# Performance work log

Measured on AMD Instinct MI355X. Metric: run time of the kernel, lower is better.

The kernel has to match this reference:

```python
import jax, jax.numpy as jnp
import numpy as np

B_, N, P, HID, KT = 1, 2048, 9, 32, 3
N_AGG = 7
AVG_LOG_DEG = 7.625  # info.deg: dataset-average log(degree+1) used by PNA scalers
EPS = 1e-8


def _adj_mats(A):
    # Precompute per-adjacency aggregation matrices (shared across b, p, c).
    mask = A > 0
    degb = jnp.maximum(jnp.sum(mask, axis=-1).astype(A.dtype), 1.0)  # [n]
    Wb = mask.astype(A.dtype) / degb[:, None]                        # binary mean
    Wa = A / (jnp.sum(A, axis=-1, keepdims=True) + EPS)              # distance-weighted mean
    neg = jnp.asarray(-1e9, A.dtype)
    Sp = jax.nn.softmax(jnp.where(mask, A, neg), axis=-1)            # softmax agg weights
    Sm = jax.nn.softmax(jnp.where(mask, -A, neg), axis=-1)           # softmin agg weights
    return Wb, Wa, Sp, Sm, degb


def spatial_conv(X, A, theta, bias, use_scalers):
    # X: [b, c, n, p]  ->  out: [b, o, n, p]
    h = jnp.transpose(X, (0, 3, 2, 1))  # [b, p, n, c]
    Wb, Wa, Sp, Sm, degb = _adj_mats(A)
    agg = lambda M, Y: jnp.einsum('nm,bpmc->bpnc', M, Y)
    h2 = h * h
    mean_b = agg(Wb, h)
    mean_a = agg(Wa, h)
    var_b = jnp.maximum(agg(Wb, h2) - mean_b * mean_b, 0.0)
    var_a = jnp.maximum(agg(Wa, h2) - mean_a * mean_a, 0.0)
    out = jnp.concatenate([
        agg(Sm, h),             # softmin
        agg(Sp, h),             # softmax
        mean_b,                 # normalized_mean
        jnp.sqrt(var_b + EPS),  # std
        var_b,                  # var
        mean_a,                 # distance
        jnp.sqrt(var_a + EPS),  # d_std
    ], axis=3)                  # [b, p, n, 7c]
    if use_scalers:
        s = (jnp.log(degb + 1.0) / AVG_LOG_DEG)[None, None, :, None]
        out = jnp.concatenate([out, out * s, out / s], axis=3)  # identity/amp/atten
    out = jnp.einsum('bpnc,co->bpno', out, theta) + bias
    out = jnp.transpose(out, (0, 3, 2, 1))  # [b, o, n, p]
    return jax.nn.leaky_relu(out, 0.01)     # dropout is a no-op at inference


def conv_t(X, w, b):
    # X: [b, c, n, p]; w: [o, i, 1, k]; 'same' padding along time dim
    y = jax.lax.conv_general_dilated(X, w, (1, 1), 'SAME',
                                     dimension_numbers=('NCHW', 'OIHW', 'NCHW'))
    return y + b[None, :, None, None]


def setup_inputs() -> dict:
    key = jax.random.key(0)
    ks = jax.random.split(key, 16)

    def xavier(k, shape):
        lim = np.sqrt(6.0 / (shape[0] + shape[1]))
        return jax.random.uniform(k, shape, jnp.float32, -lim, lim)

    stdv = 1.0 / np.sqrt(HID)
    return {
        'X': jax.random.normal(ks[0], (B_, 1, N, P), jnp.float32),
        'A_first': jax.random.uniform(ks[1], (N, N), jnp.float32),
        'A_sub': jax.random.uniform(ks[2], (N, N), jnp.float32),
        'coords': jax.random.uniform(ks[3], (N, 2), jnp.float32),
        'theta0': xavier(ks[4], (N_AGG * 1 * 1, HID)),
        'bias0': jax.random.uniform(ks[5], (HID,), jnp.float32, -stdv, stdv),
        'tconv0_w': jax.random.normal(ks[6], (2 * HID, HID, 1, KT), jnp.float32) * 0.05,
        'tconv0_b': jnp.zeros((2 * HID,), jnp.float32),
        'theta1': xavier(ks[7], (N_AGG * 3 * HID, HID)),
        'bias1': jax.random.uniform(ks[8], (HID,), jnp.float32, -stdv, stdv),
        'tconv1_w': jax.random.normal(ks[9], (HID, HID, 1, KT), jnp.float32) * 0.05,
        'tconv1_b': jnp.zeros((HID,), jnp.float32),
        'out_conv_w': jax.random.normal(ks[10], (1, HID, 1, 1), jnp.float32) * 0.1,
        'out_conv_b': jnp.zeros((1,), jnp.float32),
        'out_lin_w': jax.random.normal(ks[11], (P, P), jnp.float32) * 0.1,  # torch Linear [out,in]
        'out_lin_b': jnp.zeros((P,), jnp.float32),
    }


def reference(X, A_first, A_sub, coords, theta0, bias0, tconv0_w, tconv0_b,
              theta1, bias1, tconv1_w, tconv1_b, out_conv_w, out_conv_b,
              out_lin_w, out_lin_b):
    # pe_size=0 -> PositionalEncoding is identity (coords unused)
    h = spatial_conv(X, A_first, theta0, bias0, use_scalers=False)  # s_conv0, scalers=['identity']
    # t_conv0: GLU temporal conv; in_size == out_size so align is identity
    o = conv_t(h, tconv0_w, tconv0_b)
    h = (o[:, :HID] + h) * jax.nn.sigmoid(o[:, HID:])
    # layers from spec 'STSTr'[2:] = 'ST'
    h = spatial_conv(h, A_sub, theta1, bias1, use_scalers=True)
    h = jax.nn.sigmoid(conv_t(h, tconv1_w, tconv1_b) + h)  # sigmoid temporal conv, align=identity
    # out_conv: 1x1 conv then Linear over time dim, then ReLU (spec ends with 'r')
    y = conv_t(h, out_conv_w, out_conv_b)                   # [b, 1, n, p]
    y = jnp.einsum('bonp,qp->bonq', y, out_lin_w) + out_lin_b
    return jax.nn.relu(y)
```

## Files before the change

### kernel.cpp

```cpp
#include <hip/hip_runtime.h>
#include <cstddef>

#define NN 2048
#define PDIM 9
#define HID 32
#define PN 18432

typedef short short8 __attribute__((ext_vector_type(8)));
typedef float f32x4 __attribute__((ext_vector_type(4)));

__device__ __forceinline__ float lrelu01(float x){ return x > 0.f ? x : 0.01f*x; }
__device__ __forceinline__ float sigmoidf_(float x){ return 1.f/(1.f + __expf(-x)); }
__device__ __forceinline__ unsigned short f2bf(float x){
  union{float f; unsigned u;} v; v.f = x;
  unsigned r = v.u + 0x7fffu + ((v.u >> 16) & 1u);
  return (unsigned short)(r >> 16);
}
__device__ __forceinline__ float bf2f(unsigned short x){
  union{unsigned u; float f;} q; q.u = ((unsigned)x) << 16; return q.f;
}
__device__ __forceinline__ void glds16(const void* g, void* l){
  __builtin_amdgcn_global_load_lds(
    (const __attribute__((address_space(1))) void*)g,
    (__attribute__((address_space(3))) void*)l, 16, 0, 0);
}

__global__ __launch_bounds__(256) void statsw_kernel(
    const float* __restrict__ A0, const float* __restrict__ A1,
    const float* __restrict__ X, const float* __restrict__ w0,
    const float* __restrict__ w1, const float* __restrict__ theta1,
    float* __restrict__ stats, unsigned short* __restrict__ W4,
    unsigned short* __restrict__ Xb, unsigned short* __restrict__ W0b,
    unsigned short* __restrict__ W1b, unsigned short* __restrict__ ThT)
{
  int b = blockIdx.x;
  int t = threadIdx.x;
  if (b >= 4096){
    int gidx = (b - 4096)*256 + t;
    if (gidx < 16384){
      int p2 = gidx >> 9, mq = gidx & 511;
      int m = mq*4;
      unsigned short v[4];
#pragma unroll
      for (int j = 0; j < 4; ++j){
        float x;
        if (p2 < 9) x = X[(size_t)(m+j)*PDIM + p2];
        else if (p2 < 18){ float h = X[(size_t)(m+j)*PDIM + (p2-9)]; x = h*h; }
        else x = 0.f;
        v[j] = f2bf(x);
      }
      *reinterpret_cast<uint2*>(Xb + (size_t)p2*NN + m) =
          *reinterpret_cast<const uint2*>(v);
    } else {
      int i = gidx - 16384;
      if (i < 8192){
        int co = i >> 7, k = i & 127;
        int kk = k >> 5, ci = k & 31;
        W0b[i] = (kk < 3) ? f2bf(w0[co*96 + ci*3 + kk]) : 0;
      } else if (i < 12288){
        int i2 = i - 8192;
        int co = i2 >> 7, k = i2 & 127;
        int kk = k >> 5, ci = k & 31;
        W1b[i2] = (kk < 3) ? f2bf(w1[co*96 + ci*3 + kk]) : 0;
      } else {
        int i3 = i - 12288;
        int o2 = i3 >> 8, k = i3 & 255;
        int g = o2 >> 5, o = o2 & 31;
        ThT[i3] = (k < 224) ? f2bf(theta1[((size_t)(g*224 + k))*32 + o]) : 0;
      }
    }
    return;
  }

  int mat = b >> 11;
  int row = b & 2047;
  const float* A = (mat == 0 ? A0 : A1) + (size_t)row * NN;

  float4 a4 = *reinterpret_cast<const float4*>(A + t*8);
  float4 b4 = *reinterpret_cast<const float4*>(A + t*8 + 4);
  float av[8] = {a4.x,a4.y,a4.z,a4.w,b4.x,b4.y,b4.z,b4.w};

  float cnt = 0.f, sum = 0.f, mp = -1e9f, mneg = -1e9f;
#pragma unroll
  for (int i = 0; i < 8; ++i){
    float x = av[i];
    bool mk = x > 0.f;
    cnt += mk ? 1.f : 0.f;
    sum += x;
    if (mk){ mp = fmaxf(mp, x); mneg = fmaxf(mneg, -x); }
  }
#pragma unroll
  for (int o = 32; o > 0; o >>= 1){
    cnt += __shfl_down(cnt, o);
    sum += __shfl_down(sum, o);
    mp   = fmaxf(mp,   __shfl_down(mp, o));
    mneg = fmaxf(mneg, __shfl_down(mneg, o));
  }
  __shared__ float rb[4][4];
  __shared__ float sst[8];
  int wid = t >> 6;
  if ((t & 63) == 0){ rb[wid][0]=cnt; rb[wid][1]=sum; rb[wid][2]=mp; rb[wid][3]=mneg; }
  __syncthreads();
  float CNT = rb[0][0]+rb[1][0]+rb[2][0]+rb[3][0];
  float SUM = rb[0][1]+rb[1][1]+rb[2][1]+rb[3][1];
  float MP  = fmaxf(fmaxf(rb[0][2],rb[1][2]), fmaxf(rb[2][2],rb[3][2]));
  float MNEG= fmaxf(fmaxf(rb[0][3],rb[1][3]), fmaxf(rb[2][3],rb[3][3]));
  __syncthreads();

  float sep = 0.f, sem = 0.f;
#pragma unroll
  for (int i = 0; i < 8; ++i){
    float x = av[i];
    if (x > 0.f){ sep += __expf(x - MP); sem += __expf(-x - MNEG); }
  }
#pragma unroll
  for (int o = 32; o > 0; o >>= 1){
    sep += __shfl_down(sep, o);
    sem += __shfl_down(sem, o);
  }
  if ((t & 63) == 0){ rb[wid][0]=sep; rb[wid][1]=sem; }
  __syncthreads();
  if (t == 0){
    float SEP = rb[0][0]+rb[1][0]+rb[2][0]+rb[3][0];
    float SEM = rb[0][1]+rb[1][1]+rb[2][1]+rb[3][1];
    float deg = fmaxf(CNT, 1.f);
    bool has = CNT > 0.5f;
    float st0 = 1.f/deg;
    float st1 = 1.f/(SUM + 1e-8f);
    float st3 = has ? 1.f/SEP : 0.f;
    float st5 = has ? 1.f/SEM : 0.f;
    float st7 = has ? 0.f : 1.f;
    float* st = stats + ((size_t)mat*NN + row)*8;
    st[0]=st0; st[1]=st1; st[2]=MP; st[3]=st3; st[4]=MNEG; st[5]=st5;
    st[6]=logf(deg + 1.f)*(1.f/7.625f); st[7]=st7;
    sst[0]=st0; sst[1]=st1; sst[2]=MP; sst[3]=st3; sst[4]=MNEG; sst[5]=st5; sst[7]=st7;
  }
  __syncthreads();
  if (mat == 1){
    float s0=sst[0], s1=sst[1], s2=sst[2], s3=sst[3], s4=sst[4], s5=sst[5], s7=sst[7];
    short8 vsm, vsp, vwb, vwa;
#pragma unroll
    for (int j = 0; j < 8; ++j){
      float a = av[j];
      bool mk = a > 0.f;
      float wb = mk ? s0 : 0.f;
      float wa = a * s1;
      float wsp, wsm;
      if (s7 != 0.f){ wsp = 1.f/2048.f; wsm = 1.f/2048.f; }
      else {
        wsp = mk ? __expf(a - s2)*s3 : 0.f;
        wsm = mk ? __expf(-a - s4)*s5 : 0.f;
      }
      vsm[j] = (short)f2bf(wsm); vsp[j] = (short)f2bf(wsp);
      vwb[j] = (short)f2bf(wb);  vwa[j] = (short)f2bf(wa);
    }
    size_t base = (size_t)row*NN + t*8;
    *reinterpret_cast<short8*>(W4 + base)                   = vsm;
    *reinterpret_cast<short8*>(W4 + base + (size_t)1*NN*NN) = vsp;
    *reinterpret_cast<short8*>(W4 + base + (size_t)2*NN*NN) = vwb;
    *reinterpret_cast<short8*>(W4 + base + (size_t)3*NN*NN) = vwa;
  }
}

__global__ __launch_bounds__(256) void g0f_kernel(
    const float* __restrict__ A0, const float* __restrict__ stats,
    const unsigned short* __restrict__ Xb, float* __restrict__ C0p)
{
  __shared__ __align__(16) char smem[20480];
  int tid = threadIdx.x;
  int lane = tid & 63, wid = tid >> 6;
  int l15 = lane & 15, hi = lane >> 4, rx = l15 & 7;
  int n0 = blockIdx.x * 32;
  int kc = blockIdx.y;
  int kbase = kc * 128;
  int r = tid >> 3, cc = tid & 7;
  int n = n0 + r;
  const float* st = stats + (size_t)n*8;
  float s0=st[0], s1=st[1], s2=st[2], s3=st[3], s4=st[4], s5=st[5], s7=st[7];
  const float* Ap = A0 + (size_t)n*NN + kbase + cc*8;
  char* wdst = smem + r*128 + ((cc ^ (r & 7)) << 4);

  size_t goffB;
  {
    int jj = tid >> 3, kc8 = tid & 7;
    goffB = (size_t)jj*NN + ((kc8 ^ (jj & 7)) << 3) + kbase;
  }
  char* dstB = smem + 16384 + wid*1024;

  int abyte[2][2], bbyte[2][2];
#pragma unroll
  for (int mf = 0; mf < 2; ++mf)
#pragma unroll
    for (int ks = 0; ks < 2; ++ks)
      abyte[mf][ks] = wid*4096 + (mf*16 + l15)*128 + (((ks*4 + hi) ^ rx) << 4);
#pragma unroll
  for (int nf = 0; nf < 2; ++nf)
#pragma unroll
    for (int ks = 0; ks < 2; ++ks)
      bbyte[nf][ks] = 16384 + (nf*16 + l15)*128 + (((ks*4 + hi) ^ rx) << 4);

  f32x4 acc[2][2];
#pragma unroll
  for (int mf = 0; mf < 2; ++mf)
#pragma unroll
    for (int nf = 0; nf < 2; ++nf) acc[mf][nf] = (f32x4){0.f,0.f,0.f,0.f};

#pragma unroll
  for (int kt = 0; kt < 2; ++kt){
    int k0 = kt*64;
    __syncthreads();
    float4 a4 = *reinterpret_cast<const float4*>(Ap + k0);
    float4 b4 = *reinterpret_cast<const float4*>(Ap + k0 + 4);
    float av[8] = {a4.x,a4.y,a4.z,a4.w,b4.x,b4.y,b4.z,b4.w};
    short8 vsm, vsp, vwb, vwa;
#pragma unroll
    for (int j = 0; j < 8; ++j){
      float a = av[j];
      bool mk = a > 0.f;
      float wb = mk ? s0 : 0.f;
      float wa = a * s1;
      float wsp, wsm;
      if (s7 != 0.f){ wsp = 1.f/2048.f; wsm = 1.f/2048.f; }
      else {
        wsp = mk ? __expf(a - s2)*s3 : 0.f;
        wsm = mk ? __expf(-a - s4)*s5 : 0.f;
      }
      vsm[j] = (short)f2bf(wsm); vsp[j] = (short)f2bf(wsp);
      vwb[j] = (short)f2bf(wb);  vwa[j] = (short)f2bf(wa);
    }
    *reinterpret_cast<short8*>(wdst)         = vsm;
    *reinterpret_cast<short8*>(wdst + 4096)  = vsp;
    *reinterpret_cast<short8*>(wdst + 8192)  = vwb;
    *reinterpret_cast<short8*>(wdst + 12288) = vwa;
    glds16(Xb + goffB + k0, dstB);
    asm volatile("s_waitcnt vmcnt(0)" ::: "memory");
    __syncthreads();

    short8 afr[2][2], bfr[2][2];
#pragma unroll
    for (int mf = 0; mf < 2; ++mf)
#pragma unroll
      for (int ks = 0; ks < 2; ++ks)
        afr[mf][ks] = *reinterpret_cast<const short8*>(smem + abyte[mf][ks]);
#pragma unroll
    for (int nf = 0; nf < 2; ++nf)
#pragma unroll
      for (int ks = 0; ks < 2; ++ks)
        bfr[nf][ks] = *reinterpret_cast<const short8*>(smem + bbyte[nf][ks]);
#pragma unroll
    for (int mf = 0; mf < 2; ++mf)
#pragma unroll
      for (int nf = 0; nf < 2; ++nf)
#pragma unroll
        for (int ks = 0; ks < 2; ++ks)
          acc[mf][nf] = __builtin_amdgcn_mfma_f32_16x16x32_bf16(
              afr[mf][ks], bfr[nf][ks], acc[mf][nf], 0, 0, 0);
  }

  float* P = C0p + ((size_t)(kc*4 + wid)*NN)*18;
#pragma unroll
  for (int mf = 0; mf < 2; ++mf){
    int row0 = n0 + mf*16 + hi*4;
#pragma unroll
    for (int nf = 0; nf < 2; ++nf){
      int col = nf*16 + l15;
      if (col < 18){
        f32x4 v = acc[mf][nf];
        float* p = P + (size_t)row0*18 + col;
        p[0] = v[0]; p[18] = v[1]; p[36] = v[2]; p[54] = v[3];
      }
    }
  }
}

#define FH0   0
#define FZ    11520
#define FCAT  11584
#define FTH   16192
#define FW0   17088
#define FY    34496
#define FHG   52928
__global__ __launch_bounds__(384) void front_kernel(
    const float* __restrict__ C0p, const float* __restrict__ th0,
    const float* __restrict__ bs0, const unsigned short* __restrict__ W0bg,
    unsigned short* __restrict__ HbT)
{
  __shared__ __align__(16) char L[63296];
  int t = threadIdx.x;
  int n0n = blockIdx.x * 16;

  if (t < 288){
    int r = t >> 1, half = t & 1;
    int n = n0n + r/9, p = r % 9;
    float g[6] = {0.f,0.f,0.f,0.f,0.f,0.f};
    const size_t MOFF = (size_t)NN*18;
    for (int kc = half*8; kc < half*8 + 8; ++kc){
      const float* P = C0p + ((size_t)(kc*4)*NN + n)*18;
      g[0] += P[p];
      g[1] += P[MOFF + p];
      g[2] += P[2*MOFF + p];
      g[3] += P[3*MOFF + p];
      g[4] += P[2*MOFF + 9 + p];
      g[5] += P[3*MOFF + 9 + p];
    }
    float* sc = reinterpret_cast<float*>(L + FY) + (size_t)(r*2 + half)*6;
#pragma unroll
    for (int i = 0; i < 6; ++i) sc[i] = g[i];
  }
  if (t < 224) reinterpret_cast<float*>(L + FTH)[t] = th0[t];
  if (t < 16) reinterpret_cast<unsigned*>(L + FZ)[t] = 0u;
  __syncthreads();

  if (t < 144){
    const float* sc = reinterpret_cast<float*>(L + FY) + (size_t)(t*2)*6;
    float g0 = sc[0]+sc[6], g1 = sc[1]+sc[7], g2 = sc[2]+sc[8];
    float g3 = sc[3]+sc[9], g4 = sc[4]+sc[10], g5 = sc[5]+sc[11];
    float* cat = reinterpret_cast<float*>(L + FCAT) + t*8;
    cat[0] = g0; cat[1] = g1; cat[2] = g2;
    float vb = fmaxf(g4 - g2*g2, 0.f);
    cat[3] = sqrtf(vb + 1e-8f); cat[4] = vb;
    cat[5] = g3;
    float va = fmaxf(g5 - g3*g3, 0.f);
    cat[6] = sqrtf(va + 1e-8f);
  }
#pragma unroll
  for (int pass = 0; pass < 3; ++pass){
    int c = t + pass*384;
    if (c < 1024){
      int co = c >> 4, k16 = c & 15;
      short8 v = *reinterpret_cast<const short8*>(W0bg + co*128 + k16*8);
      *reinterpret_cast<short8*>(L + FW0 + co*272 + k16*16) = v;
    }
  }
  __syncthreads();

#pragma unroll
  for (int pass = 0; pass < 12; ++pass){
    int idx = t + pass*384;
    int r = idx >> 5, o = idx & 31;
    const float* cat = reinterpret_cast<float*>(L + FCAT) + r*8;
    const float* th = reinterpret_cast<float*>(L + FTH);
    float v = bs0[o];
#pragma unroll
    for (int a = 0; a < 7; ++a) v += cat[a]*th[a*32 + o];
    *reinterpret_cast<unsigned short*>(L + FH0 + r*80 + o*2) = f2bf(lrelu01(v));
  }
  __syncthreads();

  int lane = t & 63, wid = t >> 6;
  int wr = wid >> 1, wc = wid & 1;
  int l15 = lane & 15, hi = lane >> 4;
  int rr[3], pp[3];
#pragma unroll
  for (int mfi = 0; mfi < 3; ++mfi){
    rr[mfi] = wr*48 + mfi*16 + l15;
    pp[mfi] = rr[mfi] % 9;
  }
  f32x4 acc[3][2];
#pragma unroll
  for (int mfi = 0; mfi < 3; ++mfi)
#pragma unroll
    for (int nf = 0; nf < 2; ++nf) acc[mfi][nf] = (f32x4){0.f,0.f,0.f,0.f};
#pragma unroll
  for (int ks = 0; ks < 4; ++ks){
    int idx16 = ks*4 + hi;
    int kk = idx16 >> 2, ci0 = (idx16 & 3)*8;
    short8 bfr[2];
#pragma unroll
    for (int nf = 0; nf < 2; ++nf){
      int col = wc*32 + nf*16 + l15;
      bfr[nf] = *reinterpret_cast<const short8*>(L + FW0 + col*272 + idx16*16);
    }
#pragma unroll
    for (int mfi = 0; mfi < 3; ++mfi){
      int pk = pp[mfi] + kk - 1;
      bool valid = (kk < 3) && ((unsigned)pk < 9u);
      int aoff = valid ? (FH0 + (rr[mfi] + kk - 1)*80 + ci0*2) : FZ;
      short8 af = *reinterpret_cast<const short8*>(L + aoff);
#pragma unroll
      for (int nf = 0; nf < 2; ++nf)
        acc[mfi][nf] = __builtin_amdgcn_mfma_f32_16x16x32_bf16(
            af, bfr[nf], acc[mfi][nf], 0, 0, 0);
    }
  }
  __syncthreads();

#pragma unroll
  for (int mfi = 0; mfi < 3; ++mfi){
    int r0 = wr*48 + mfi*16 + hi*4;
#pragma unroll
    for (int nf = 0; nf < 2; ++nf){
      int col = wc*32 + nf*16 + l15;
      f32x4 v = acc[mfi][nf];
      unsigned short* e = reinterpret_cast<unsigned short*>(L + FY) + (size_t)r0*64 + col;
      e[0] = f2bf(v[0]); e[64] = f2bf(v[1]); e[128] = f2bf(v[2]); e[192] = f2bf(v[3]);
    }
  }
  __syncthreads();

#pragma unroll
  for (int pass = 0; pass < 12; ++pass){
    int idx = t + pass*384;
    int r = idx >> 5, c = idx & 31;
    const unsigned short* Y = reinterpret_cast<unsigned short*>(L + FY) + (size_t)r*64;
    float h = bf2f(*reinterpret_cast<unsigned short*>(L + FH0 + r*80 + c*2));
    float v = (bf2f(Y[c]) + h) * sigmoidf_(bf2f(Y[32 + c]));
    reinterpret_cast<unsigned short*>(L + FHG)[(size_t)r*36 + c] = f2bf(v);
  }
  __syncthreads();

#pragma unroll
  for (int pass = 0; pass < 3; ++pass){
    int job = t + pass*384;
    int j2h = job >> 1, half = job & 1;
    int sq = (j2h >= 288);
    int j = sq ? j2h - 288 : j2h;
    int p = j >> 5, c = j & 31;
    unsigned short v[8];
#pragma unroll
    for (int mi = 0; mi < 8; ++mi){
      int r = (half*8 + mi)*9 + p;
      float x = bf2f(reinterpret_cast<unsigned short*>(L + FHG)[(size_t)r*36 + c]);
      if (sq) x = x*x;
      v[mi] = f2bf(x);
    }
    *reinterpret_cast<short8*>(HbT + (size_t)j2h*NN + n0n + half*8) =
        *reinterpret_cast<const short8*>(v);
  }
}

__global__ __launch_bounds__(256) void gemm2_kernel(
    const unsigned short* __restrict__ W4, const unsigned short* __restrict__ HbT,
    unsigned short* __restrict__ catb)
{
  __shared__ __align__(16) char smem[49152];
  int tid = threadIdx.x;
  int lane = tid & 63, wid = tid >> 6;
  int wr = wid >> 1, wc = wid & 1;
  int l15 = lane & 15, hi = lane >> 4, rx = l15 & 7;

  int bid = blockIdx.x;
  int xcd = bid & 7, slot = bid >> 3;
  int pl = slot / 9, q = slot - pl*9;
  int panel = xcd*8 + pl;
  int a = panel >> 4;
  int n0 = (panel & 15) * 128;
  bool need2 = (a >= 2);

  const unsigned short* Wa = W4 + (size_t)a*NN*NN + (size_t)n0*NN;

  size_t goffA[4];
#pragma unroll
  for (int i = 0; i < 4; ++i){
    int chunk = i*256 + tid;
    int r = chunk >> 3, cc = chunk & 7;
    goffA[i] = (size_t)r*NN + ((cc ^ (r & 7)) << 3);
  }
  size_t goffB1, goffB2;
  {
    int jj = tid >> 3, kc = tid & 7;
    goffB1 = (size_t)(32*q + jj)*NN + ((kc ^ (jj & 7)) << 3);
    goffB2 = goffB1 + (size_t)288*NN;
  }

  int abyte[4][2], bbyte[2][2];
#pragma unroll
  for (int mf = 0; mf < 4; ++mf)
#pragma unroll
    for (int ks = 0; ks < 2; ++ks)
      abyte[mf][ks] = (wr*64 + mf*16 + l15)*128 + (((ks*4 + hi) ^ rx) << 4);
#pragma unroll
  for (int nf = 0; nf < 2; ++nf)
#pragma unroll
    for (int ks = 0; ks < 2; ++ks)
      bbyte[nf][ks] = 16384 + (wc*32 + nf*16 + l15)*128 + (((ks*4 + hi) ^ rx) << 4);

  f32x4 acc[4][2];
#pragma unroll
  for (int mf = 0; mf < 4; ++mf)
#pragma unroll
    for (int nf = 0; nf < 2; ++nf) acc[mf][nf] = (f32x4){0.f,0.f,0.f,0.f};

  bool mywork = need2 || (wc == 0);

#define STAGE2(bufoff, kk) do { \
    _Pragma("unroll") \
    for (int i = 0; i < 4; ++i) \
      glds16(Wa + goffA[i] + (kk), smem + (bufoff) + i*4096 + wid*1024); \
    glds16(HbT + goffB1 + (kk), smem + (bufoff) + 16384 + wid*1024); \
    if (need2) glds16(HbT + goffB2 + (kk), smem + (bufoff) + 20480 + wid*1024); \
  } while(0)

  STAGE2(0, 0);

  int cur = 0;
  for (int kt = 0; kt < 32; ++kt){
    int co = cur*24576;
    if (kt < 31){
      STAGE2(co ^ 24576, (kt+1)*64);
      if (need2) asm volatile("s_waitcnt vmcnt(6)" ::: "memory");
      else       asm volatile("s_waitcnt vmcnt(5)" ::: "memory");
    } else {
      asm volatile("s_waitcnt vmcnt(0)" ::: "memory");
    }
    __builtin_amdgcn_s_barrier();
    if (mywork){
      short8 afr[4][2], bfr[2][2];
#pragma unroll
      for (int mf = 0; mf < 4; ++mf)
#pragma unroll
        for (int ks = 0; ks < 2; ++ks)
          afr[mf][ks] = *reinterpret_cast<const short8*>(smem + co + abyte[mf][ks]);
#pragma unroll
      for (int nf = 0; nf < 2; ++nf)
#pragma unroll
        for (int ks = 0; ks < 2; ++ks)
          bfr[nf][ks] = *reinterpret_cast<const short8*>(smem + co + bbyte[nf][ks]);
#pragma unroll
      for (int mf = 0; mf < 4; ++mf)
#pragma unroll
        for (int nf = 0; nf < 2; ++nf)
#pragma unroll
          for (int ks = 0; ks < 2; ++ks)
            acc[mf][nf] = __builtin_amdgcn_mfma_f32_16x16x32_bf16(
                afr[mf][ks], bfr[nf][ks], acc[mf][nf], 0, 0, 0);
    }
    __builtin_amdgcn_s_barrier();
    cur ^= 1;
  }
#undef STAGE2

  __syncthreads();
  float* Ep = reinterpret_cast<float*>(smem);
  if (mywork){
#pragma unroll
    for (int mf = 0; mf < 4; ++mf){
      int r0 = wr*64 + mf*16 + hi*4;
#pragma unroll
      for (int nf = 0; nf < 2; ++nf){
        int col = nf*16 + l15;
        f32x4 v = acc[mf][nf];
        float* e = Ep + wc*4096 + r0*32 + col;
        e[0] = v[0]; e[32] = v[1]; e[64] = v[2]; e[96] = v[3];
      }
    }
  }
  __syncthreads();
  {
    int col = tid & 31, rb2 = tid >> 5;
#pragma unroll
    for (int i = 0; i < 16; ++i){
      int r = rb2 + 8*i;
      size_t pn = (size_t)(n0 + r)*PDIM + q;
      unsigned short* base = catb + pn*256;
      float m = Ep[r*32 + col];
      if (a == 0){
        base[col] = f2bf(m);
        base[224 + col] = 0;
      } else if (a == 1){
        base[32 + col] = f2bf(m);
      } else if (a == 2){
        float hh = Ep[4096 + r*32 + col];
        float vb = fmaxf(hh - m*m, 0.f);
        base[64 + col]  = f2bf(m);
        base[96 + col]  = f2bf(sqrtf(vb + 1e-8f));
        base[128 + col] = f2bf(vb);
      } else {
        float hh = Ep[4096 + r*32 + col];
        float va = fmaxf(hh - m*m, 0.f);
        base[160 + col] = f2bf(m);
        base[192 + col] = f2bf(sqrtf(va + 1e-8f));
      }
    }
  }
}

#define TBUF  0
#define TH1   30720
#define TW1   42240
#define TZ    50944
#define TYL   51008
__global__ __launch_bounds__(384) void tail_kernel(
    const unsigned short* __restrict__ catb, const unsigned short* __restrict__ ThT,
    const float* __restrict__ stats1, const float* __restrict__ bias1,
    const unsigned short* __restrict__ W1bg,
    const float* __restrict__ ocw, const float* __restrict__ ocb,
    const float* __restrict__ olw, const float* __restrict__ olb,
    float* __restrict__ out)
{
  __shared__ __align__(16) char L[51584];
  int t = threadIdx.x;
  int lane = t & 63, wid = t >> 6;
  int wr = wid >> 1, wc = wid & 1;
  int l15 = lane & 15, hi = lane >> 4, rx = l15 & 7;
  int n0n = blockIdx.x * 16;
  int rowbase = n0n * 9;

#pragma unroll
  for (int pass = 0; pass < 2; ++pass){
    int c = t + pass*384;
    if (c < 512){
      int co = c >> 4, k16 = c & 15;
      short8 v = *reinterpret_cast<const short8*>(W1bg + co*128 + k16*8);
      *reinterpret_cast<short8*>(L + TW1 + co*272 + k16*16) = v;
    }
  }
  if (t < 16) reinterpret_cast<unsigned*>(L + TZ)[t] = 0u;

  size_t goffA[3];
#pragma unroll
  for (int i = 0; i < 3; ++i){
    int el = (wid*3 + i)*64 + lane;
    int r = el >> 3, cc = el & 7;
    goffA[i] = (size_t)(rowbase + r)*256 + ((cc ^ (r & 7)) << 3);
  }
  size_t goffB[2];
#pragma unroll
  for (int i = 0; i < 2; ++i){
    int el = (wid*2 + i)*64 + lane;
    int j = el >> 3, kc = el & 7;
    goffB[i] = (size_t)j*256 + ((kc ^ (j & 7)) << 3);
  }

  int abyte[3][2], bbyte[3][2];
#pragma unroll
  for (int mfi = 0; mfi < 3; ++mfi)
#pragma unroll
    for (int ks = 0; ks < 2; ++ks)
      abyte[mfi][ks] = (wr*48 + mfi*16 + l15)*128 + (((ks*4 + hi) ^ rx) << 4);
#pragma unroll
  for (int nf = 0; nf < 3; ++nf)
#pragma unroll
    for (int ks = 0; ks < 2; ++ks)
      bbyte[nf][ks] = 18432 + (wc*48 + nf*16 + l15)*128 + (((ks*4 + hi) ^ rx) << 4);

  f32x4 acc[3][3];
#pragma unroll
  for (int mfi = 0; mfi < 3; ++mfi)
#pragma unroll
    for (int nf = 0; nf < 3; ++nf) acc[mfi][nf] = (f32x4){0.f,0.f,0.f,0.f};

  for (int kt = 0; kt < 4; ++kt){
    int k0 = kt*64;
    __syncthreads();
#pragma unroll
    for (int i = 0; i < 3; ++i)
      glds16(catb + goffA[i] + k0, L + (wid*3 + i)*1024);
#pragma unroll
    for (int i = 0; i < 2; ++i)
      glds16(ThT + goffB[i] + k0, L + 18432 + (wid*2 + i)*1024);
    asm volatile("s_waitcnt vmcnt(0)" ::: "memory");
    __syncthreads();

    short8 afr[3][2], bfr[3][2];
#pragma unroll
    for (int mfi = 0; mfi < 3; ++mfi)
#pragma unroll
      for (int ks = 0; ks < 2; ++ks)
        afr[mfi][ks] = *reinterpret_cast<const short8*>(L + abyte[mfi][ks]);
#pragma unroll
    for (int nf = 0; nf < 3; ++nf)
#pragma unroll
      for (int ks = 0; ks < 2; ++ks)
        bfr[nf][ks] = *reinterpret_cast<const short8*>(L + bbyte[nf][ks]);
#pragma unroll
    for (int mfi = 0; mfi < 3; ++mfi)
#pragma unroll
      for (int nf = 0; nf < 3; ++nf)
#pragma unroll
        for (int ks = 0; ks < 2; ++ks)
          acc[mfi][nf] = __builtin_amdgcn_mfma_f32_16x16x32_bf16(
              afr[mfi][ks], bfr[nf][ks], acc[mfi][nf], 0, 0, 0);
  }
  __syncthreads();

#pragma unroll
  for (int mfi = 0; mfi < 3; ++mfi){
    int r0 = wr*48 + mfi*16 + hi*4;
#pragma unroll
    for (int nf = 0; nf < 3; ++nf){
      int col = wc*48 + nf*16 + l15;
      f32x4 v = acc[mfi][nf];
      unsigned short* e = reinterpret_cast<unsigned short*>(L + TBUF) + (size_t)r0*96 + col;
      e[0] = f2bf(v[0]); e[96] = f2bf(v[1]); e[192] = f2bf(v[2]); e[288] = f2bf(v[3]);
    }
  }
  __syncthreads();

#pragma unroll
  for (int pass = 0; pass < 12; ++pass){
    int idx = t + pass*384;
    int r = idx >> 5, o = idx & 31;
    int n = n0n + r/9;
    float s = stats1[(size_t)n*8 + 6];
    float inv = 1.f / s;
    const unsigned short* Y = reinterpret_cast<unsigned short*>(L + TBUF) + (size_t)r*96;
    float v = bias1[o] + bf2f(Y[o]) + s*bf2f(Y[32 + o]) + inv*bf2f(Y[64 + o]);
    *reinterpret_cast<unsigned short*>(L + TH1 + r*80 + o*2) = f2bf(lrelu01(v));
  }
  __syncthreads();

  int rr[3], pp[3];
#pragma unroll
  for (int mfi = 0; mfi < 3; ++mfi){
    rr[mfi] = wr*48 + mfi*16 + l15;
    pp[mfi] = rr[mfi] % 9;
  }
  f32x4 acc2[3];
#pragma unroll
  for (int mfi = 0; mfi < 3; ++mfi) acc2[mfi] = (f32x4){0.f,0.f,0.f,0.f};
  int colc = wc*16 + l15;
#pragma unroll
  for (int ks = 0; ks < 4; ++ks){
    int idx16 = ks*4 + hi;
    int kk = idx16 >> 2, ci0 = (idx16 & 3)*8;
    short8 bf = *reinterpret_cast<const short8*>(L + TW1 + colc*272 + idx16*16);
#pragma unroll
    for (int mfi = 0; mfi < 3; ++mfi){
      int pk = pp[mfi] + kk - 1;
      bool valid = (kk < 3) && ((unsigned)pk < 9u);
      int aoff = valid ? (TH1 + (rr[mfi] + kk - 1)*80 + ci0*2) : TZ;
      short8 af = *reinterpret_cast<const short8*>(L + aoff);
      acc2[mfi] = __builtin_amdgcn_mfma_f32_16x16x32_bf16(af, bf, acc2[mfi], 0, 0, 0);
    }
  }
  __syncthreads();

#pragma unroll
  for (int mfi = 0; mfi < 3; ++mfi){
    int r0 = wr*48 + mfi*16 + hi*4;
    f32x4 v = acc2[mfi];
#pragma unroll
    for (int i = 0; i < 4; ++i){
      int r = r0 + i;
      float h = bf2f(*reinterpret_cast<unsigned short*>(L + TH1 + r*80 + colc*2));
      reinterpret_cast<float*>(L + TBUF)[(size_t)r*36 + colc] = sigmoidf_(v[i] + h);
    }
  }
  __syncthreads();

  if (t < 144){
    float y = ocb[0];
    const float* hs = reinterpret_cast<float*>(L + TBUF) + (size_t)t*36;
#pragma unroll
    for (int c = 0; c < 32; ++c) y += ocw[c]*hs[c];
    reinterpret_cast<float*>(L + TYL)[t] = y;
  }
  __syncthreads();
  if (t < 144){
    int n_l = t / 9, q = t % 9;
    const float* yl = reinterpret_cast<float*>(L + TYL) + n_l*9;
    float accv = olb[q];
#pragma unroll
    for (int p = 0; p < 9; ++p) accv += yl[p]*olw[q*9 + p];
    out[(size_t)(n0n + n_l)*9 + q] = fmaxf(accv, 0.f);
  }
}

extern "C" void kernel_launch(void* const* d_in, const int* in_sizes, int n_in,
                              void* d_out, int out_size, void* d_ws, size_t ws_size,
                              hipStream_t stream)
{
  const float* X   = (const float*)d_in[0];
  const float* A0  = (const float*)d_in[1];
  const float* A1  = (const float*)d_in[2];
  const float* th0 = (const float*)d_in[4];
  const float* bs0 = (const float*)d_in[5];
  const float* w0  = (const float*)d_in[6];
  const float* th1 = (const float*)d_in[8];
  const float* bs1 = (const float*)d_in[9];
  const float* w1  = (const float*)d_in[10];
  const float* ocw = (const float*)d_in[12];
  const float* ocb = (const float*)d_in[13];
  const float* olw = (const float*)d_in[14];
  const float* olb = (const float*)d_in[15];
  float* out = (float*)d_out;
  float* ws  = (float*)d_ws;

  float* stats = ws;
  unsigned short* Xb   = (unsigned short*)(ws + 32768);
  float* C0p           = ws + 65536;
  unsigned short* catb = (unsigned short*)(ws + 65536);
  unsigned short* W4   = (unsigned short*)(ws + 2424832);
  unsigned short* HbT  = (unsigned short*)(ws + 10813440);
  unsigned short* W0b  = (unsigned short*)(ws + 11403264);
  unsigned short* W1b  = (unsigned short*)(ws + 11407360);
  unsigned short* ThT  = (unsigned short*)(ws + 11409408);

  hipLaunchKernelGGL(statsw_kernel,dim3(4304), dim3(256), 0, stream,
                     A0, A1, X, w0, w1, th1, stats, W4, Xb, W0b, W1b, ThT);
  hipLaunchKernelGGL(g0f_kernel,   dim3(64,16),dim3(256), 0, stream, A0, stats, Xb, C0p);
  hipLaunchKernelGGL(front_kernel, dim3(128),  dim3(384), 0, stream, C0p, th0, bs0, W0b, HbT);
  hipLaunchKernelGGL(gemm2_kernel, dim3(576),  dim3(256), 0, stream, W4, HbT, catb);
  hipLaunchKernelGGL(tail_kernel,  dim3(128),  dim3(384), 0, stream,
                     catb, ThT, stats + 16384, bs1, W1b, ocw, ocb, olw, olb, out);
}
```

Before: 77.68 us.

## Pair two time-step columns per block for single-output aggregations in gemm2

```diff
diff --git a/kernel.cpp b/kernel.cpp
--- a/kernel.cpp
+++ b/kernel.cpp
@@ -441,11 +441,20 @@
 
   int bid = blockIdx.x;
   int xcd = bid & 7, slot = bid >> 3;
-  int pl = slot / 9, q = slot - pl*9;
-  int panel = xcd*8 + pl;
+  int panel, q, q2;
+  if (slot < 20){
+    int pl = slot / 5, qp = slot % 5;
+    panel = xcd*4 + pl;
+    q = qp*2; q2 = (qp == 4) ? 8 : qp*2 + 1;
+  } else {
+    int s2 = slot - 20;
+    int pl = s2 / 9;
+    panel = 32 + xcd*4 + pl;
+    q = s2 % 9; q2 = q;
+  }
   int a = panel >> 4;
   int n0 = (panel & 15) * 128;
-  bool need2 = (a >= 2);
+  bool alo = (a < 2);
 
   const unsigned short* Wa = W4 + (size_t)a*NN*NN + (size_t)n0*NN;
 
@@ -459,8 +468,10 @@
   size_t goffB1, goffB2;
   {
     int jj = tid >> 3, kc = tid & 7;
-    goffB1 = (size_t)(32*q + jj)*NN + ((kc ^ (jj & 7)) << 3);
-    goffB2 = goffB1 + (size_t)288*NN;
+    int sw = ((kc ^ (jj & 7)) << 3);
+    goffB1 = (size_t)(32*q + jj)*NN + sw;
+    goffB2 = alo ? ((size_t)(32*q2 + jj)*NN + sw)
+                 : (goffB1 + (size_t)288*NN);
   }
 
   int abyte[4][2], bbyte[2][2];
@@ -480,15 +491,13 @@
   for (int mf = 0; mf < 4; ++mf)
 #pragma unroll
     for (int nf = 0; nf < 2; ++nf) acc[mf][nf] = (f32x4){0.f,0.f,0.f,0.f};
-
-  bool mywork = need2 || (wc == 0);
 
 #define STAGE2(bufoff, kk) do { \
     _Pragma("unroll") \
     for (int i = 0; i < 4; ++i) \
       glds16(Wa + goffA[i] + (kk), smem + (bufoff) + i*4096 + wid*1024); \
     glds16(HbT + goffB1 + (kk), smem + (bufoff) + 16384 + wid*1024); \
-    if (need2) glds16(HbT + goffB2 + (kk), smem + (bufoff) + 20480 + wid*1024); \
+    glds16(HbT + goffB2 + (kk), smem + (bufoff) + 20480 + wid*1024); \
   } while(0)
 
   STAGE2(0, 0);
@@ -498,13 +507,12 @@
     int co = cur*24576;
     if (kt < 31){
       STAGE2(co ^ 24576, (kt+1)*64);
-      if (need2) asm volatile("s_waitcnt vmcnt(6)" ::: "memory");
-      else       asm volatile("s_waitcnt vmcnt(5)" ::: "memory");
+      asm volatile("s_waitcnt vmcnt(6)" ::: "memory");
     } else {
       asm volatile("s_waitcnt vmcnt(0)" ::: "memory");
     }
     __builtin_amdgcn_s_barrier();
-    if (mywork){
+    {
       short8 afr[4][2], bfr[2][2];
 #pragma unroll
       for (int mf = 0; mf < 4; ++mf)
@@ -532,7 +540,7 @@
 
   __syncthreads();
   float* Ep = reinterpret_cast<float*>(smem);
-  if (mywork){
+  {
 #pragma unroll
     for (int mf = 0; mf < 4; ++mf){
       int r0 = wr*64 + mf*16 + hi*4;
@@ -554,20 +562,28 @@
       size_t pn = (size_t)(n0 + r)*PDIM + q;
       unsigned short* base = catb + pn*256;
       float m = Ep[r*32 + col];
+      float m2 = Ep[4096 + r*32 + col];
       if (a == 0){
         base[col] = f2bf(m);
         base[224 + col] = 0;
+        if (q2 != q){
+          unsigned short* b2 = catb + ((size_t)(n0 + r)*PDIM + q2)*256;
+          b2[col] = f2bf(m2);
+          b2[224 + col] = 0;
+        }
       } else if (a == 1){
         base[32 + col] = f2bf(m);
+        if (q2 != q){
+          unsigned short* b2 = catb + ((size_t)(n0 + r)*PDIM + q2)*256;
+          b2[32 + col] = f2bf(m2);
+        }
       } else if (a == 2){
-        float hh = Ep[4096 + r*32 + col];
-        float vb = fmaxf(hh - m*m, 0.f);
+        float vb = fmaxf(m2 - m*m, 0.f);
         base[64 + col]  = f2bf(m);
         base[96 + col]  = f2bf(sqrtf(vb + 1e-8f));
         base[128 + col] = f2bf(vb);
       } else {
-        float hh = Ep[4096 + r*32 + col];
-        float va = fmaxf(hh - m*m, 0.f);
+        float va = fmaxf(m2 - m*m, 0.f);
         base[160 + col] = f2bf(m);
         base[192 + col] = f2bf(sqrtf(va + 1e-8f));
       }
@@ -791,7 +807,7 @@
                      A0, A1, X, w0, w1, th1, stats, W4, Xb, W0b, W1b, ThT);
   hipLaunchKernelGGL(g0f_kernel,   dim3(64,16),dim3(256), 0, stream, A0, stats, Xb, C0p);
   hipLaunchKernelGGL(front_kernel, dim3(128),  dim3(384), 0, stream, C0p, th0, bs0, W0b, HbT);
-  hipLaunchKernelGGL(gemm2_kernel, dim3(576),  dim3(256), 0, stream, W4, HbT, catb);
+  hipLaunchKernelGGL(gemm2_kernel, dim3(448),  dim3(256), 0, stream, W4, HbT, catb);
   hipLaunchKernelGGL(tail_kernel,  dim3(128),  dim3(384), 0, stream,
                      catb, ThT, stats + 16384, bs1, W1b, ocw, ocb, olw, olb, out);
 }
```

Result: faster. 71.45 us, median of 2 (-8.0%).
